# Kernel optimization log

Hardware: AMD Instinct MI355X
Metric: run time of the kernel (lower is better)

The kernel has to match this reference:

```python
import jax, jax.numpy as jnp
import numpy as np

N_NODES = 50000


def setup_inputs() -> dict:
    key = jax.random.key(0)
    k = jax.random.split(key, 5)
    x = jax.random.normal(k[0], (N_NODES, 64), dtype=jnp.float32)
    edge_index = jax.random.randint(k[1], (2, 800000), 0, N_NODES, dtype=jnp.int64)
    # Glorot-ish init for weights
    W1 = jax.random.normal(k[2], (64, 64), dtype=jnp.float32) * (1.0 / np.sqrt(64))
    b1 = jnp.zeros((64,), dtype=jnp.float32)
    W2 = jax.random.normal(k[3], (64, 16), dtype=jnp.float32) * (1.0 / np.sqrt(64))
    b2 = jnp.zeros((16,), dtype=jnp.float32)
    return {"x": x, "edge_index": edge_index, "W1": W1, "b1": b1, "W2": W2, "b2": b2}


def _gcn_conv(h, row, col, W, b, n_nodes):
    # PyG GCNConv: add self-loops, symmetric deg normalization, linear, scatter-add.
    h = h @ W                                   # [N, out]
    deg = jax.ops.segment_sum(jnp.ones_like(col, dtype=h.dtype), col,
                              num_segments=n_nodes)          # in-degree incl. self-loops
    dinv = jnp.where(deg > 0, jax.lax.rsqrt(deg), 0.0)       # deg^{-1/2}
    norm = dinv[row] * dinv[col]                             # [E]
    msg = h[row] * norm[:, None]                             # gather + scale, [E, out]
    out = jax.ops.segment_sum(msg, col, num_segments=n_nodes)  # scatter-add at targets
    return out + b


def reference(x, edge_index, W1, b1, W2, b2):
    n = x.shape[0]
    loops = jnp.arange(n, dtype=edge_index.dtype)
    row = jnp.concatenate([edge_index[0], loops])  # sources (with self-loops)
    col = jnp.concatenate([edge_index[1], loops])  # targets (with self-loops)
    h = _gcn_conv(x, row, col, W1, b1, n)
    h = jax.nn.relu(h)
    h = _gcn_conv(h, row, col, W2, b2, n)
    return jax.nn.log_softmax(h, axis=1)
```

## Files before the change

kernel.cpp:

```cpp
#include <hip/hip_runtime.h>
#include <hip/hip_bf16.h>
#include <math.h>


#define BLK 256
#define EPB 4096
#define GSH 7
#define GMASK 127
#define GMAX 512
#define QCAP 3072

typedef __attribute__((ext_vector_type(8))) short short8;
typedef __attribute__((ext_vector_type(4))) float float4v;
typedef __attribute__((ext_vector_type(4))) unsigned short ushort4v;

__device__ __forceinline__ short f2bf(float f) {
    __hip_bfloat16 h = __float2bfloat16(f);
    union { __hip_bfloat16 h; short s; } u; u.h = h; return u.s;
}
__device__ __forceinline__ float bf2f(short s) {
    union { short s; __hip_bfloat16 h; } u; u.s = s; return __bfloat162float(u.h);
}
__device__ __forceinline__ float ldf(const void* p, long long i, int f32) {
    if (f32) return ((const float*)p)[i];
    return __bfloat162float(((const __hip_bfloat16*)p)[i]);
}
__device__ __forceinline__ float4v mfma_bf16(short8 a, short8 b, float4v c) {
    return __builtin_amdgcn_mfma_f32_16x16x32_bf16(a, b, c, 0, 0, 0);
}

__global__ void init_k(const void* edge_raw, const unsigned short* xraw, long long n_nodes,
                       const void* W1, const void* W2, const void* b1, const void* b2,
                       int* flags, short* wT1, short* wT2, float* b1f, float* b2f,
                       int* gtail, int G) {
    __shared__ int bad, cnt;
    int tid = threadIdx.x;
    if (tid == 0) { bad = 0; cnt = 0; }
    __syncthreads();
    const long long* p = (const long long*)edge_raw;
    for (int i = tid; i < 1024; i += BLK) {
        long long v = p[i];
        if (v < 0 || v >= n_nodes) bad = 1;
    }
    int e = (xraw[2 * tid] >> 7) & 0xFF;
    int inr = (e >= 96 && e <= 130) ? 1 : 0;
    __syncthreads();
    if (inr) atomicAdd(&cnt, 1);
    __syncthreads();
    int f32 = (cnt < 128) ? 1 : 0;
    if (tid == 0) { flags[0] = bad ? 0 : 1; flags[1] = f32; }
    for (int i = tid; i < G * 16; i += BLK) gtail[i] = 0;
    for (int idx = tid; idx < 4096; idx += BLK) {
        int k = idx >> 6, j = idx & 63;
        wT1[j * 64 + k] = f2bf(ldf(W1, idx, f32));
    }
    for (int idx = tid; idx < 1024; idx += BLK) {
        int k = idx >> 4, j = idx & 15;
        wT2[j * 64 + k] = f2bf(ldf(W2, idx, f32));
    }
    if (tid < 64) b1f[tid] = ldf(b1, tid, f32);
    if (tid < 16) b2f[tid] = ldf(b2, tid, f32);
}

__global__ __launch_bounds__(BLK) void binAmm1_k(const void* edge_raw, const void* x,
                                                 const int* __restrict__ flags, int E,
                                                 int* gtail, int* __restrict__ queue,
                                                 const short* __restrict__ wT1,
                                                 unsigned short* __restrict__ h1,
                                                 int N, int G, int nblkA) {
    int bid = blockIdx.x, tid = threadIdx.x;
    if (bid < nblkA) {
        __shared__ int hist[GMAX], base[GMAX];
        for (int g = tid; g < G; g += BLK) hist[g] = 0;
        __syncthreads();
        int is64 = flags[0];
        int e0 = bid * EPB;
        int r[16], c[16], pos[16];
        const long long* p64 = (const long long*)edge_raw;
        const int* p32 = (const int*)edge_raw;
        #pragma unroll
        for (int i = 0; i < 16; ++i) {
            int e = e0 + i * BLK + tid;
            int rr = -1, cc = 0;
            if (e < E) {
                if (is64) { rr = (int)p64[e]; cc = (int)p64[(long long)E + e]; }
                else      { rr = p32[e];      cc = p32[E + e]; }
            }
            r[i] = rr; c[i] = cc;
            pos[i] = (rr >= 0) ? atomicAdd(&hist[cc >> GSH], 1) : 0;
        }
        __syncthreads();
        for (int g = tid; g < G; g += BLK) {
            int h = hist[g];
            base[g] = h ? atomicAdd(&gtail[g << 4], h) : 0;
        }
        __syncthreads();
        #pragma unroll
        for (int i = 0; i < 16; ++i) {
            if (r[i] >= 0) {
                int g = c[i] >> GSH;
                int idx = base[g] + pos[i];
                if (idx < QCAP)
                    queue[(long long)g * QCAP + idx] = (r[i] << GSH) | (c[i] & GMASK);
            }
        }
    } else {
        int wave = ((bid - nblkA) << 2) + (tid >> 6);
        int lane = tid & 63;
        int node0 = wave << 4;
        if (node0 >= N) return;
        int m = lane & 15, quad = lane >> 4;
        int node = node0 + m;
        int nc = node < N ? node : N - 1;
        short8 a0, a1;
        if (flags[1]) {
            const float* xf = (const float*)x + ((long long)nc << 6) + quad * 8;
            #pragma unroll
            for (int i = 0; i < 8; ++i) { a0[i] = f2bf(xf[i]); a1[i] = f2bf(xf[32 + i]); }
        } else {
            const unsigned short* xb = (const unsigned short*)x + ((long long)nc << 6) + quad * 8;
            a0 = *(const short8*)xb;
            a1 = *(const short8*)(xb + 32);
        }
        const short8* wp = (const short8*)wT1;
        #pragma unroll
        for (int jt = 0; jt < 4; ++jt) {
            float4v cc = {0.f, 0.f, 0.f, 0.f};
            cc = mfma_bf16(a0, wp[((jt * 16 + m) << 3) + quad], cc);
            cc = mfma_bf16(a1, wp[((jt * 16 + m) << 3) + 4 + quad], cc);
            #pragma unroll
            for (int r2 = 0; r2 < 4; ++r2) {
                int n2 = node0 + (quad << 2) + r2;
                if (n2 < N) h1[((long long)n2 << 6) + jt * 16 + m] = (unsigned short)f2bf(cc[r2]);
            }
        }
    }
}

__global__ __launch_bounds__(1024) void binB_k(const int* __restrict__ gtail,
                                               const int* __restrict__ queue,
                                               unsigned short* __restrict__ srcs,
                                               int* __restrict__ cntf,
                                               float* __restrict__ dinv, int N) {
    __shared__ int lcnt[128];
    int g = blockIdx.x, tid = threadIdx.x;
    if (tid < 128) lcnt[tid] = 0;
    __syncthreads();
    int len = gtail[g << 4];
    if (len > QCAP) len = QCAP;
    const int* q = queue + (long long)g * QCAP;
    int n0 = g << GSH;
    for (int i = tid; i < len; i += 1024) {
        int u = q[i];
        int cl = u & GMASK, rr = u >> GSH;
        int pos = atomicAdd(&lcnt[cl], 1);
        if (pos < 64) srcs[((long long)(n0 + cl) << 6) + pos] = (unsigned short)rr;
    }
    __syncthreads();
    if (tid < 128) {
        int gn = n0 + tid;
        if (gn < N) {
            cntf[gn] = lcnt[tid];
            dinv[gn] = rsqrtf((float)lcnt[tid] + 1.0f);
        }
    }
}

__global__ __launch_bounds__(BLK) void agg1mm2_k(const unsigned short* __restrict__ h1,
                                                 const int* __restrict__ cntf,
                                                 const float* __restrict__ dinv,
                                                 const unsigned short* __restrict__ srcs,
                                                 const short* __restrict__ wT2,
                                                 const float* __restrict__ b1f,
                                                 unsigned short* __restrict__ h2, int N) {
    __shared__ short a_lds[16][72];
    int b = blockIdx.x, tid = threadIdx.x;
    int wv = tid >> 6, lane = tid & 63;
    #pragma unroll
    for (int k = 0; k < 4; ++k) {
        int nl = wv * 4 + k;
        int gn = (b << 4) + nl;
        float acc = 0.f, dc = 1.f;
        if (gn < N) {
            int dg = cntf[gn];
            int m = dg < 64 ? dg : 64;
            const unsigned short* sp = srcs + ((long long)gn << 6);
            dc = dinv[gn];
            acc = bf2f((short)h1[((long long)gn << 6) + lane]) * dc;
            int e = 0;
            for (; e + 7 < m; e += 8) {
                ushort4v qa = *(const ushort4v*)(sp + e);
                ushort4v qb = *(const ushort4v*)(sp + e + 4);
                int r0 = qa[0], r1 = qa[1], r2 = qa[2], r3 = qa[3];
                int r4 = qb[0], r5 = qb[1], r6 = qb[2], r7 = qb[3];
                float f0 = bf2f((short)h1[((long long)r0 << 6) + lane]);
                float f1 = bf2f((short)h1[((long long)r1 << 6) + lane]);
                float f2v = bf2f((short)h1[((long long)r2 << 6) + lane]);
                float f3 = bf2f((short)h1[((long long)r3 << 6) + lane]);
                float f4 = bf2f((short)h1[((long long)r4 << 6) + lane]);
                float f5 = bf2f((short)h1[((long long)r5 << 6) + lane]);
                float f6 = bf2f((short)h1[((long long)r6 << 6) + lane]);
                float f7 = bf2f((short)h1[((long long)r7 << 6) + lane]);
                float d0 = dinv[r0], d1 = dinv[r1], d2 = dinv[r2], d3 = dinv[r3];
                float d4 = dinv[r4], d5 = dinv[r5], d6 = dinv[r6], d7 = dinv[r7];
                acc += (f0 * d0 + f1 * d1 + f2v * d2 + f3 * d3)
                     + (f4 * d4 + f5 * d5 + f6 * d6 + f7 * d7);
            }
            for (; e + 3 < m; e += 4) {
                ushort4v q = *(const ushort4v*)(sp + e);
                int r0 = q[0], r1 = q[1], r2 = q[2], r3 = q[3];
                float d0 = dinv[r0], d1 = dinv[r1], d2 = dinv[r2], d3 = dinv[r3];
                float f0 = bf2f((short)h1[((long long)r0 << 6) + lane]);
                float f1 = bf2f((short)h1[((long long)r1 << 6) + lane]);
                float f2v = bf2f((short)h1[((long long)r2 << 6) + lane]);
                float f3 = bf2f((short)h1[((long long)r3 << 6) + lane]);
                acc += f0 * d0 + f1 * d1 + f2v * d2 + f3 * d3;
            }
            for (; e < m; ++e) {
                int r = sp[e];
                acc += bf2f((short)h1[((long long)r << 6) + lane]) * dinv[r];
            }
        }
        float hg = acc * dc;
        a_lds[nl][lane] = f2bf(fmaxf(hg + b1f[lane], 0.f));
    }
    __syncthreads();
    if (wv == 0) {
        int m = lane & 15, quad = lane >> 4;
        short8 a0 = *(const short8*)&a_lds[m][quad * 8];
        short8 a1 = *(const short8*)&a_lds[m][quad * 8 + 32];
        const short8* wp = (const short8*)wT2;
        float4v c = {0.f, 0.f, 0.f, 0.f};
        c = mfma_bf16(a0, wp[(m << 3) + quad], c);
        c = mfma_bf16(a1, wp[(m << 3) + 4 + quad], c);
        #pragma unroll
        for (int r = 0; r < 4; ++r) {
            int n2 = (b << 4) + (quad << 2) + r;
            if (n2 < N) h2[((long long)n2 << 4) + m] = (unsigned short)f2bf(c[r] * dinv[n2]);
        }
    }
}

__global__ __launch_bounds__(BLK) void agg2sm_k(const unsigned short* __restrict__ h2,
                                                const int* __restrict__ cntf,
                                                const unsigned short* __restrict__ srcs,
                                                const float* __restrict__ b2f,
                                                const int* __restrict__ flags,
                                                void* __restrict__ out, int N) {
    int c = (blockIdx.x * BLK + threadIdx.x) >> 6;
    if (c >= N) return;
    int lane = threadIdx.x & 63;
    int eo = lane >> 4, j = lane & 15;
    int dg = cntf[c];
    int m = dg < 64 ? dg : 64;
    const unsigned short* sp = srcs + ((long long)c << 6);
    float acc = 0.f;
    int e = eo;
    for (; e + 4 < m; e += 8) {
        float va = bf2f((short)h2[((long long)sp[e] << 4) + j]);
        float vb = bf2f((short)h2[((long long)sp[e + 4] << 4) + j]);
        acc += va + vb;
    }
    for (; e < m; e += 4)
        acc += bf2f((short)h2[((long long)sp[e] << 4) + j]);
    acc += __shfl_xor(acc, 16, 64);
    acc += __shfl_xor(acc, 32, 64);
    float selfv = bf2f((short)h2[((long long)c << 4) + j]);
    float logit = (acc + selfv) * rsqrtf((float)dg + 1.0f) + b2f[j];
    float mx = logit;
    mx = fmaxf(mx, __shfl_xor(mx, 1, 64));
    mx = fmaxf(mx, __shfl_xor(mx, 2, 64));
    mx = fmaxf(mx, __shfl_xor(mx, 4, 64));
    mx = fmaxf(mx, __shfl_xor(mx, 8, 64));
    float s = expf(logit - mx);
    s += __shfl_xor(s, 1, 64);
    s += __shfl_xor(s, 2, 64);
    s += __shfl_xor(s, 4, 64);
    s += __shfl_xor(s, 8, 64);
    float res = logit - mx - logf(s);
    if (eo == 0) {
        if (flags[1]) ((float*)out)[((long long)c << 4) + j] = res;
        else ((__hip_bfloat16*)out)[((long long)c << 4) + j] = __float2bfloat16(res);
    }
}

extern "C" void kernel_launch(void* const* d_in, const int* in_sizes, int n_in,
                              void* d_out, int out_size, void* d_ws, size_t ws_size,
                              hipStream_t stream) {
    const void* x        = d_in[0];
    const void* edge_raw = d_in[1];
    const void* W1       = d_in[2];
    const void* b1       = d_in[3];
    const void* W2       = d_in[4];
    const void* b2       = d_in[5];

    const int N = in_sizes[0] / 64;
    const int E = in_sizes[1] / 2;
    const int G = (N + GMASK) >> GSH;

    char* ws = (char*)d_ws;
    size_t o = 0;
    auto take = [&](size_t bytes) { char* p = ws + o; o += (bytes + 255) & ~(size_t)255; return p; };
    int*            flags  = (int*)take(256);
    int*            gtail  = (int*)take((size_t)G * 64);
    int*            queue  = (int*)take((size_t)G * QCAP * 4);
    unsigned short* srcs   = (unsigned short*)take((size_t)N * 64 * 2);
    int*            cntf   = (int*)take((size_t)N * 4);
    float*          dinv   = (float*)take((size_t)N * 4);
    float*          b1f    = (float*)take(64 * 4);
    float*          b2f    = (float*)take(16 * 4);
    short*          wT1    = (short*)take(4096 * 2);
    short*          wT2    = (short*)take(1024 * 2);
    unsigned short* h1     = (unsigned short*)take((size_t)N * 64 * 2);
    unsigned short* h2     = (unsigned short*)take((size_t)N * 16 * 2);

    int nblkA = (E + EPB - 1) / EPB;
    int nblkW = ((N + 15) / 16 + 3) / 4;
    int NBUCK = (N + 15) / 16;
    int nblkG = ((size_t)N * 64 + BLK - 1) / BLK;

    init_k<<<1, BLK, 0, stream>>>(edge_raw, (const unsigned short*)x, (long long)N,
                                  W1, W2, b1, b2, flags, wT1, wT2, b1f, b2f, gtail, G);
    binAmm1_k<<<nblkA + nblkW, BLK, 0, stream>>>(edge_raw, x, flags, E, gtail, queue,
                                                 wT1, h1, N, G, nblkA);
    binB_k<<<G, 1024, 0, stream>>>(gtail, queue, srcs, cntf, dinv, N);
    agg1mm2_k<<<NBUCK, BLK, 0, stream>>>(h1, cntf, dinv, srcs, wT2, b1f, h2, N);
    agg2sm_k<<<nblkG, BLK, 0, stream>>>(h2, cntf, srcs, b2f, flags, d_out, N);
}
```

Before: 156.0 us.

## Prescale h1 by source dinv in binB and drop per-edge dinv gathers

binB_k now multiplies each row of h1 by its own deg^-1/2 once after counting degrees, so the layer-1 aggregation no longer gathers dinv per edge and only sums prescaled features. The aggregation loops in agg1mm2_k and agg2sm_k are unrolled further (16 and 32 edges per step) to keep more gathers in flight. init_k spreads zeroing of gtail across 64 blocks instead of one. The trade-off is an extra read-modify-write pass over h1 and a second bf16 rounding of the prescaled values.

```diff
diff --git a/kernel.cpp b/kernel.cpp
--- a/kernel.cpp
+++ b/kernel.cpp
@@ -33,8 +33,10 @@
                        const void* W1, const void* W2, const void* b1, const void* b2,
                        int* flags, short* wT1, short* wT2, float* b1f, float* b2f,
                        int* gtail, int G) {
+    int tid = threadIdx.x, bid = blockIdx.x;
+    for (int i = bid * BLK + tid; i < G * 16; i += gridDim.x * BLK) gtail[i] = 0;
+    if (bid != 0) return;
     __shared__ int bad, cnt;
-    int tid = threadIdx.x;
     if (tid == 0) { bad = 0; cnt = 0; }
     __syncthreads();
     const long long* p = (const long long*)edge_raw;
@@ -49,7 +51,6 @@
     __syncthreads();
     int f32 = (cnt < 128) ? 1 : 0;
     if (tid == 0) { flags[0] = bad ? 0 : 1; flags[1] = f32; }
-    for (int i = tid; i < G * 16; i += BLK) gtail[i] = 0;
     for (int idx = tid; idx < 4096; idx += BLK) {
         int k = idx >> 6, j = idx & 63;
         wT1[j * 64 + k] = f2bf(ldf(W1, idx, f32));
@@ -141,7 +142,8 @@
                                                const int* __restrict__ queue,
                                                unsigned short* __restrict__ srcs,
                                                int* __restrict__ cntf,
-                                               float* __restrict__ dinv, int N) {
+                                               float* __restrict__ dinv,
+                                               unsigned short* __restrict__ h1, int N) {
     __shared__ int lcnt[128];
     int g = blockIdx.x, tid = threadIdx.x;
     if (tid < 128) lcnt[tid] = 0;
@@ -162,6 +164,19 @@
         if (gn < N) {
             cntf[gn] = lcnt[tid];
             dinv[gn] = rsqrtf((float)lcnt[tid] + 1.0f);
+        }
+    }
+    {
+        int row = tid >> 3, sgi = tid & 7;
+        int gn = n0 + row;
+        if (gn < N) {
+            float dv = rsqrtf((float)lcnt[row] + 1.0f);
+            unsigned short* hp = h1 + ((long long)gn << 6) + (sgi << 3);
+            short8 v = *(const short8*)hp;
+            short8 o2;
+            #pragma unroll
+            for (int i = 0; i < 8; ++i) o2[i] = f2bf(bf2f(v[i]) * dv);
+            *(short8*)hp = o2;
         }
     }
 }
@@ -186,39 +201,56 @@
             int m = dg < 64 ? dg : 64;
             const unsigned short* sp = srcs + ((long long)gn << 6);
             dc = dinv[gn];
-            acc = bf2f((short)h1[((long long)gn << 6) + lane]) * dc;
+            acc = bf2f((short)h1[((long long)gn << 6) + lane]);
             int e = 0;
+            for (; e + 15 < m; e += 16) {
+                ushort4v q0 = *(const ushort4v*)(sp + e);
+                ushort4v q1 = *(const ushort4v*)(sp + e + 4);
+                ushort4v q2 = *(const ushort4v*)(sp + e + 8);
+                ushort4v q3 = *(const ushort4v*)(sp + e + 12);
+                float f0 = bf2f((short)h1[((long long)q0[0] << 6) + lane]);
+                float f1 = bf2f((short)h1[((long long)q0[1] << 6) + lane]);
+                float f2 = bf2f((short)h1[((long long)q0[2] << 6) + lane]);
+                float f3 = bf2f((short)h1[((long long)q0[3] << 6) + lane]);
+                float f4 = bf2f((short)h1[((long long)q1[0] << 6) + lane]);
+                float f5 = bf2f((short)h1[((long long)q1[1] << 6) + lane]);
+                float f6 = bf2f((short)h1[((long long)q1[2] << 6) + lane]);
+                float f7 = bf2f((short)h1[((long long)q1[3] << 6) + lane]);
+                float f8 = bf2f((short)h1[((long long)q2[0] << 6) + lane]);
+                float f9 = bf2f((short)h1[((long long)q2[1] << 6) + lane]);
+                float fa = bf2f((short)h1[((long long)q2[2] << 6) + lane]);
+                float fb = bf2f((short)h1[((long long)q2[3] << 6) + lane]);
+                float fc = bf2f((short)h1[((long long)q3[0] << 6) + lane]);
+                float fd = bf2f((short)h1[((long long)q3[1] << 6) + lane]);
+                float fe = bf2f((short)h1[((long long)q3[2] << 6) + lane]);
+                float ff = bf2f((short)h1[((long long)q3[3] << 6) + lane]);
+                acc += (((f0 + f1) + (f2 + f3)) + ((f4 + f5) + (f6 + f7)))
+                     + (((f8 + f9) + (fa + fb)) + ((fc + fd) + (fe + ff)));
+            }
             for (; e + 7 < m; e += 8) {
-                ushort4v qa = *(const ushort4v*)(sp + e);
-                ushort4v qb = *(const ushort4v*)(sp + e + 4);
-                int r0 = qa[0], r1 = qa[1], r2 = qa[2], r3 = qa[3];
-                int r4 = qb[0], r5 = qb[1], r6 = qb[2], r7 = qb[3];
-                float f0 = bf2f((short)h1[((long long)r0 << 6) + lane]);
-                float f1 = bf2f((short)h1[((long long)r1 << 6) + lane]);
-                float f2v = bf2f((short)h1[((long long)r2 << 6) + lane]);
-                float f3 = bf2f((short)h1[((long long)r3 << 6) + lane]);
-                float f4 = bf2f((short)h1[((long long)r4 << 6) + lane]);
-                float f5 = bf2f((short)h1[((long long)r5 << 6) + lane]);
-                float f6 = bf2f((short)h1[((long long)r6 << 6) + lane]);
-                float f7 = bf2f((short)h1[((long long)r7 << 6) + lane]);
-                float d0 = dinv[r0], d1 = dinv[r1], d2 = dinv[r2], d3 = dinv[r3];
-                float d4 = dinv[r4], d5 = dinv[r5], d6 = dinv[r6], d7 = dinv[r7];
-                acc += (f0 * d0 + f1 * d1 + f2v * d2 + f3 * d3)
-                     + (f4 * d4 + f5 * d5 + f6 * d6 + f7 * d7);
+                ushort4v q0 = *(const ushort4v*)(sp + e);
+                ushort4v q1 = *(const ushort4v*)(sp + e + 4);
+                float f0 = bf2f((short)h1[((long long)q0[0] << 6) + lane]);
+                float f1 = bf2f((short)h1[((long long)q0[1] << 6) + lane]);
+                float f2 = bf2f((short)h1[((long long)q0[2] << 6) + lane]);
+                float f3 = bf2f((short)h1[((long long)q0[3] << 6) + lane]);
+                float f4 = bf2f((short)h1[((long long)q1[0] << 6) + lane]);
+                float f5 = bf2f((short)h1[((long long)q1[1] << 6) + lane]);
+                float f6 = bf2f((short)h1[((long long)q1[2] << 6) + lane]);
+                float f7 = bf2f((short)h1[((long long)q1[3] << 6) + lane]);
+                acc += ((f0 + f1) + (f2 + f3)) + ((f4 + f5) + (f6 + f7));
             }
             for (; e + 3 < m; e += 4) {
-                ushort4v q = *(const ushort4v*)(sp + e);
-                int r0 = q[0], r1 = q[1], r2 = q[2], r3 = q[3];
-                float d0 = dinv[r0], d1 = dinv[r1], d2 = dinv[r2], d3 = dinv[r3];
-                float f0 = bf2f((short)h1[((long long)r0 << 6) + lane]);
-                float f1 = bf2f((short)h1[((long long)r1 << 6) + lane]);
-                float f2v = bf2f((short)h1[((long long)r2 << 6) + lane]);
-                float f3 = bf2f((short)h1[((long long)r3 << 6) + lane]);
-                acc += f0 * d0 + f1 * d1 + f2v * d2 + f3 * d3;
+                ushort4v q0 = *(const ushort4v*)(sp + e);
+                float f0 = bf2f((short)h1[((long long)q0[0] << 6) + lane]);
+                float f1 = bf2f((short)h1[((long long)q0[1] << 6) + lane]);
+                float f2 = bf2f((short)h1[((long long)q0[2] << 6) + lane]);
+                float f3 = bf2f((short)h1[((long long)q0[3] << 6) + lane]);
+                acc += (f0 + f1) + (f2 + f3);
             }
             for (; e < m; ++e) {
                 int r = sp[e];
-                acc += bf2f((short)h1[((long long)r << 6) + lane]) * dinv[r];
+                acc += bf2f((short)h1[((long long)r << 6) + lane]);
             }
         }
         float hg = acc * dc;
@@ -256,6 +288,24 @@
     const unsigned short* sp = srcs + ((long long)c << 6);
     float acc = 0.f;
     int e = eo;
+    for (; e + 28 < m; e += 32) {
+        float v0 = bf2f((short)h2[((long long)sp[e]      << 4) + j]);
+        float v1 = bf2f((short)h2[((long long)sp[e + 4]  << 4) + j]);
+        float v2 = bf2f((short)h2[((long long)sp[e + 8]  << 4) + j]);
+        float v3 = bf2f((short)h2[((long long)sp[e + 12] << 4) + j]);
+        float v4 = bf2f((short)h2[((long long)sp[e + 16] << 4) + j]);
+        float v5 = bf2f((short)h2[((long long)sp[e + 20] << 4) + j]);
+        float v6 = bf2f((short)h2[((long long)sp[e + 24] << 4) + j]);
+        float v7 = bf2f((short)h2[((long long)sp[e + 28] << 4) + j]);
+        acc += ((v0 + v1) + (v2 + v3)) + ((v4 + v5) + (v6 + v7));
+    }
+    for (; e + 12 < m; e += 16) {
+        float v0 = bf2f((short)h2[((long long)sp[e]      << 4) + j]);
+        float v1 = bf2f((short)h2[((long long)sp[e + 4]  << 4) + j]);
+        float v2 = bf2f((short)h2[((long long)sp[e + 8]  << 4) + j]);
+        float v3 = bf2f((short)h2[((long long)sp[e + 12] << 4) + j]);
+        acc += (v0 + v1) + (v2 + v3);
+    }
     for (; e + 4 < m; e += 8) {
         float va = bf2f((short)h2[((long long)sp[e] << 4) + j]);
         float vb = bf2f((short)h2[((long long)sp[e + 4] << 4) + j]);
@@ -319,11 +369,11 @@
     int NBUCK = (N + 15) / 16;
     int nblkG = ((size_t)N * 64 + BLK - 1) / BLK;
 
-    init_k<<<1, BLK, 0, stream>>>(edge_raw, (const unsigned short*)x, (long long)N,
-                                  W1, W2, b1, b2, flags, wT1, wT2, b1f, b2f, gtail, G);
+    init_k<<<64, BLK, 0, stream>>>(edge_raw, (const unsigned short*)x, (long long)N,
+                                   W1, W2, b1, b2, flags, wT1, wT2, b1f, b2f, gtail, G);
     binAmm1_k<<<nblkA + nblkW, BLK, 0, stream>>>(edge_raw, x, flags, E, gtail, queue,
                                                  wT1, h1, N, G, nblkA);
-    binB_k<<<G, 1024, 0, stream>>>(gtail, queue, srcs, cntf, dinv, N);
+    binB_k<<<G, 1024, 0, stream>>>(gtail, queue, srcs, cntf, dinv, h1, N);
     agg1mm2_k<<<NBUCK, BLK, 0, stream>>>(h1, cntf, dinv, srcs, wT2, b1f, h2, N);
     agg2sm_k<<<nblkG, BLK, 0, stream>>>(h2, cntf, srcs, b2f, flags, d_out, N);
 }
```

Result: faster. 152.4 us (median of 2 runs) (-2.3%).
